# Kernel tuning notes

Hardware: AMD Instinct MI355X
Metric: run time of the kernel (lower is better)

The kernel has to match this reference:

```python
import jax, jax.numpy as jnp
import numpy as np

D_MODEL = 768
NHEAD = 12
HEAD_DIM = D_MODEL // NHEAD
B, L = 8, 1024


def setup_inputs() -> dict:
    key = jax.random.key(0)
    ks = jax.random.split(key, 10)
    s = 0.02  # init scale for weights
    return {
        "x": jax.random.normal(ks[0], (B, L, D_MODEL), dtype=jnp.float32),
        "pos": jax.random.normal(ks[1], (B, L, D_MODEL), dtype=jnp.float32),
        "qkv_w": jax.random.normal(ks[2], (3 * D_MODEL, D_MODEL), dtype=jnp.float32) * s,
        "qkv_b": jnp.zeros((3 * D_MODEL,), dtype=jnp.float32),
        "pq_w": jax.random.normal(ks[3], (D_MODEL, D_MODEL), dtype=jnp.float32) * s,
        "pq_b": jnp.zeros((D_MODEL,), dtype=jnp.float32),
        "pk_w": jax.random.normal(ks[4], (D_MODEL, D_MODEL), dtype=jnp.float32) * s,
        "pk_b": jnp.zeros((D_MODEL,), dtype=jnp.float32),
    }


def reference(x, pos, qkv_w, qkv_b, pq_w, pq_b, pk_w, pk_b):
    b, l, d = x.shape
    h, hd = NHEAD, HEAD_DIM

    qkv = x @ qkv_w.T + qkv_b  # (b, l, 3d)
    q, k, v = jnp.split(qkv, 3, axis=-1)
    # rearrange 'b l (h d) -> b l h d'
    q = q.reshape(b, l, h, hd)
    k = k.reshape(b, l, h, hd)
    v = v.reshape(b, l, h, hd)

    pq = (pos @ pq_w.T + pq_b).reshape(b, l, h, hd)
    pk = (pos @ pk_w.T + pk_b).reshape(b, l, h, hd)

    CC = jnp.einsum('bnhd,blhd->bhnl', q, k)
    CP = jnp.einsum('bnhd,blhd->bhnl', q, pq)
    PC = jnp.einsum('bnhd,blhd->bhnl', k, pk)

    # Faithful to source: only PC is scaled (operator precedence in original)
    scale = (3 * d) ** 0.5
    attn = jax.nn.softmax(CC + CP + PC / scale, axis=-1)

    out = jnp.einsum('bhnl,blhd->bnhd', attn, v)  # (b, n, h, hd)
    return out
```

## Files before the change

kernel.cpp:

```cpp
#include <hip/hip_runtime.h>
#include <hip/hip_bf16.h>

#define NHEAD 12
#define BATCH 8
#define SEQ 1024
#define LOG2E 1.4426950408889634f

typedef __bf16 bf16x8 __attribute__((ext_vector_type(8)));
typedef float  f32x4  __attribute__((ext_vector_type(4)));

#define WAITVM0 asm volatile("s_waitcnt vmcnt(0)" ::: "memory")

#define MFMA(A, B, C) __builtin_amdgcn_mfma_f32_16x16x32_bf16(A, B, C, 0, 0, 0)

__device__ __forceinline__ unsigned short f2bf(float f) {
    union { float f; unsigned u; } v; v.f = f;
    unsigned u = v.u;
    u += 0x7fff + ((u >> 16) & 1);
    return (unsigned short)(u >> 16);
}

__device__ __forceinline__ unsigned pkbf(float a, float b) {
    union { __hip_bfloat162 h; unsigned u; } cv;
    cv.h = __float22bfloat162_rn(make_float2(a, b));
    return cv.u;
}

__device__ __forceinline__ void gload_lds16(const void* g, void* l) {
    __builtin_amdgcn_global_load_lds(
        (const __attribute__((address_space(1))) unsigned*)g,
        (__attribute__((address_space(3))) unsigned*)l, 16, 0, 0);
}

#define SZ_X    6291456
#define SZ_QKVW 1769472
#define SZ_PW   589824
#define CONV_TOTAL 15532032

__global__ __launch_bounds__(256) void convert_kernel(
    const float* __restrict__ x, const float* __restrict__ pos,
    const float* __restrict__ qkv_w, const float* __restrict__ pq_w,
    const float* __restrict__ pk_w, unsigned short* __restrict__ dst)
{
    const size_t i4 = ((size_t)blockIdx.x * 256 + threadIdx.x) * 4;
    if (i4 >= CONV_TOTAL) return;
    const float* src; size_t off;
    if (i4 < SZ_X)                { src = x;     off = i4; }
    else if (i4 < 2 * SZ_X)       { src = pos;   off = i4 - SZ_X; }
    else if (i4 < 2 * SZ_X + SZ_QKVW) { src = qkv_w; off = i4 - 2 * SZ_X; }
    else if (i4 < 2 * SZ_X + SZ_QKVW + SZ_PW) { src = pq_w; off = i4 - 2 * SZ_X - SZ_QKVW; }
    else                          { src = pk_w;  off = i4 - 2 * SZ_X - SZ_QKVW - SZ_PW; }
    float4 v = *(const float4*)(src + off);
    ushort4 o;
    o.x = f2bf(v.x); o.y = f2bf(v.y); o.z = f2bf(v.z); o.w = f2bf(v.w);
    *(ushort4*)(dst + i4) = o;
}


#define PROJ_STAGE(K0, AS, BS) do {                                          \
    const int k0_ = (K0);                                                    \
    const unsigned short* asrc_; int acol_;                                  \
    if (g == 4)                    { asrc_ = posb; acol_ = k0_; }            \
    else if (g == 3 && k0_ >= 768) { asrc_ = posb; acol_ = k0_ - 768; }      \
    else                           { asrc_ = xb;   acol_ = k0_; }            \
    gload_lds16(asrc_ + (size_t)(m0 + r0) * 768 + acol_ + q0 * 8, &AS[base0]);\
    gload_lds16(asrc_ + (size_t)(m0 + r1) * 768 + acol_ + q1 * 8, &AS[base1]);\
    const unsigned short* wsrc_; int wro_, wco_;                             \
    if (g <= 2)       { wsrc_ = qkvw; wro_ = n0;        wco_ = k0_; }        \
    else if (g == 3) {                                                       \
        if (k0_ < 768) { wsrc_ = qkvw; wro_ = n0 - 1536; wco_ = k0_; }       \
        else           { wsrc_ = pqw;  wro_ = n0 - 2304; wco_ = k0_ - 768; } \
    } else            { wsrc_ = pkw;  wro_ = n0 - 3072; wco_ = k0_; }        \
    gload_lds16(wsrc_ + (size_t)(wro_ + r0) * 768 + wco_ + q0 * 8, &BS[base0]);\
    gload_lds16(wsrc_ + (size_t)(wro_ + r1) * 768 + wco_ + q1 * 8, &BS[base1]);\
} while (0)

#define PROJ_COMPUTE(AS, BS) do {                                            \
    bf16x8 af[4], bfr[4];                                                    \
    _Pragma("unroll")                                                        \
    for (int mt = 0; mt < 4; ++mt) {                                         \
        const int rr = wm + mt * 16 + col16;                                 \
        af[mt] = *(const bf16x8*)&AS[rr * 32 + ((quad ^ ((rr >> 1) & 3)) * 8)];\
    }                                                                        \
    _Pragma("unroll")                                                        \
    for (int nt = 0; nt < 4; ++nt) {                                         \
        const int rr = wn + nt * 16 + col16;                                 \
        bfr[nt] = *(const bf16x8*)&BS[rr * 32 + ((quad ^ ((rr >> 1) & 3)) * 8)];\
    }                                                                        \
    _Pragma("unroll")                                                        \
    for (int mt = 0; mt < 4; ++mt)                                           \
        _Pragma("unroll")                                                    \
        for (int nt = 0; nt < 4; ++nt)                                       \
            acc[mt][nt] = MFMA(af[mt], bfr[nt], acc[mt][nt]);                \
} while (0)

__global__ __launch_bounds__(256, 3) void proj_kernel(
    const unsigned short* __restrict__ xb, const unsigned short* __restrict__ posb,
    const unsigned short* __restrict__ qkvw, const unsigned short* __restrict__ pqw,
    const unsigned short* __restrict__ pkw,
    const float* __restrict__ qkv_b, const float* __restrict__ pq_b,
    const float* __restrict__ pk_b,
    unsigned short* __restrict__ Q2, unsigned short* __restrict__ K2,
    unsigned short* __restrict__ Vt, int band)
{
    __shared__ unsigned short As0[128 * 32];
    __shared__ unsigned short As1[128 * 32];
    __shared__ unsigned short Bs0[128 * 32];
    __shared__ unsigned short Bs1[128 * 32];

    const int id  = blockIdx.x;
    const int xcd = id & 7;
    const int idx = id >> 3;
    const int nt30 = (idx / band + 18) % 30;
    const int m0 = (xcd * band + idx % band) * 128;
    const int n0 = nt30 * 128;
    const int g  = n0 / 768;
    const int nk = (g == 3) ? 48 : 24;

    const int tid   = threadIdx.x;
    const int lane  = tid & 63;
    const int w     = tid >> 6;
    const int wm    = (w & 1) * 64;
    const int wn    = (w >> 1) * 64;
    const int quad  = lane >> 4;
    const int col16 = lane & 15;

    const int c0 = w * 64 + lane;
    const int c1 = c0 + 256;
    const int r0 = c0 >> 2, q0 = (c0 & 3) ^ ((c0 >> 3) & 3);
    const int r1 = c1 >> 2, q1 = (c1 & 3) ^ ((c1 >> 3) & 3);
    const int base0 = (w * 64) * 8;
    const int base1 = (w * 64 + 256) * 8;

    f32x4 acc[4][4];
    const f32x4 fzero = {0.f, 0.f, 0.f, 0.f};
#pragma unroll
    for (int mt = 0; mt < 4; ++mt)
#pragma unroll
        for (int nt = 0; nt < 4; ++nt) acc[mt][nt] = fzero;

    PROJ_STAGE(0, As0, Bs0);

    for (int kt = 0; kt < nk; kt += 2) {
        WAITVM0;
        __syncthreads();
        PROJ_STAGE((kt + 1) * 32, As1, Bs1);
        PROJ_COMPUTE(As0, Bs0);

        WAITVM0;
        __syncthreads();
        if (kt + 2 < nk) PROJ_STAGE((kt + 2) * 32, As0, Bs0);
        PROJ_COMPUTE(As1, Bs1);
    }

#pragma unroll
    for (int mt = 0; mt < 4; ++mt) {
        const int mbase = m0 + wm + mt * 16 + quad * 4;
#pragma unroll
        for (int nt = 0; nt < 4; ++nt) {
            const int n = n0 + wn + nt * 16 + col16;
            if (g == 2) {
                const int b = mbase >> 10, l0 = mbase & 1023;
                const int c = n - 1536, h = c >> 6, dd = c & 63;
                const float bias = qkv_b[n];
                uint2 pk;
                pk.x = pkbf(acc[mt][nt][0] + bias, acc[mt][nt][1] + bias);
                pk.y = pkbf(acc[mt][nt][2] + bias, acc[mt][nt][3] + bias);
                *(uint2*)&Vt[((size_t)(b * NHEAD + h) * 64 + dd) * 1024 + l0] = pk;
                continue;
            }
#pragma unroll
            for (int r = 0; r < 4; ++r) {
                const int m = mbase + r;
                const int b = m >> 10, l = m & 1023;
                float val = acc[mt][nt][r];
                if (g == 0) {
                    val = (val + qkv_b[n]) * LOG2E;
                    const int h = n >> 6, dd = n & 63;
                    Q2[((size_t)(b * NHEAD + h) * 1024 + l) * 128 + dd] = f2bf(val);
                } else if (g == 1) {
                    val = (val + qkv_b[n]) * (LOG2E / 48.0f);
                    const int c = n - 768, h = c >> 6, dd = c & 63;
                    Q2[((size_t)(b * NHEAD + h) * 1024 + l) * 128 + 64 + dd] = f2bf(val);
                } else if (g == 3) {
                    const int c = n - 2304;
                    val += qkv_b[n - 1536] + pq_b[c];
                    const int h = c >> 6, dd = c & 63;
                    K2[((size_t)(b * NHEAD + h) * 1024 + l) * 128 + dd] = f2bf(val);
                } else {
                    const int c = n - 3072;
                    val += pk_b[c];
                    const int h = c >> 6, dd = c & 63;
                    K2[((size_t)(b * NHEAD + h) * 1024 + l) * 128 + 64 + dd] = f2bf(val);
                }
            }
        }
    }
}


#define ATTN_STG(J0, KS, VS) do {                                            \
    const int j0_ = (J0);                                                    \
    gload_lds16(&K2[q2base + (size_t)(j0_ + kr0) * 128 + kc0 * 8], &KS[kbase0]);\
    gload_lds16(&K2[q2base + (size_t)(j0_ + kr1) * 128 + kc1 * 8], &KS[kbase1]);\
    gload_lds16(&Vt[vtbase + (size_t)vr * 1024 + j0_ + vc * 8],    &VS[vbase]);\
} while (0)

#define ATTN_PV(VS, PSR) do {                                                \
    bf16x8 bp0 = *(const bf16x8*)&PSR[w][col16][quad * 8];                   \
    bf16x8 bp1 = *(const bf16x8*)&PSR[w][16 + col16][quad * 8];              \
    _Pragma("unroll")                                                        \
    for (int c2 = 0; c2 < 4; ++c2) {                                         \
        const int rv = c2 * 16 + col16;                                      \
        bf16x8 av = *(const bf16x8*)&VS[rv * 32 + ((quad ^ ((rv >> 2) & 3)) * 8)];\
        o[0][c2] = MFMA(av, bp0, o[0][c2]);                                  \
        o[1][c2] = MFMA(av, bp1, o[1][c2]);                                  \
    }                                                                        \
} while (0)

#define ATTN_QK(KS, PSW) do {                                                \
    f32x4 st[2][2] = {{fzero, fzero}, {fzero, fzero}};                       \
    _Pragma("unroll")                                                        \
    for (int kk = 0; kk < 4; ++kk) {                                         \
        const int rrj0 = col16, rrj1 = 16 + col16;                           \
        bf16x8 kf0 = *(const bf16x8*)&KS[rrj0 * 128 + (((kk * 4 + quad) ^ (rrj0 & 15)) * 8)];\
        bf16x8 kf1 = *(const bf16x8*)&KS[rrj1 * 128 + (((kk * 4 + quad) ^ (rrj1 & 15)) * 8)];\
        _Pragma("unroll")                                                    \
        for (int qt = 0; qt < 2; ++qt) {                                     \
            st[0][qt] = MFMA(kf0, bq[qt][kk], st[0][qt]);                    \
            st[1][qt] = MFMA(kf1, bq[qt][kk], st[1][qt]);                    \
        }                                                                    \
    }                                                                        \
    _Pragma("unroll")                                                        \
    for (int qt = 0; qt < 2; ++qt) {                                         \
        float p0[4], p1[4], s = 0.f;                                         \
        _Pragma("unroll")                                                    \
        for (int r = 0; r < 4; ++r) {                                        \
            p0[r] = __builtin_amdgcn_exp2f(st[0][qt][r]);                    \
            p1[r] = __builtin_amdgcn_exp2f(st[1][qt][r]);                    \
            s += p0[r] + p1[r];                                              \
        }                                                                    \
        lsum[qt] += s;                                                       \
        uint2 w0, w1;                                                        \
        w0.x = pkbf(p0[0], p0[1]); w0.y = pkbf(p0[2], p0[3]);                \
        w1.x = pkbf(p1[0], p1[1]); w1.y = pkbf(p1[2], p1[3]);                \
        *(uint2*)&PSW[w][qt * 16 + col16][quad * 4]      = w0;               \
        *(uint2*)&PSW[w][qt * 16 + col16][16 + quad * 4] = w1;               \
    }                                                                        \
} while (0)

#define ATTN_PHASE(J, KQK, KST, VPV, VST, PSW, PSR, DOPV, DOST) do {         \
    WAITVM0;                                                                 \
    __syncthreads();                                                         \
    if (DOST) ATTN_STG(((J) + 1) * 32, KST, VST);                            \
    if (DOPV) ATTN_PV(VPV, PSR);                                             \
    ATTN_QK(KQK, PSW);                                                       \
} while (0)

__global__ __launch_bounds__(256, 3) void attn_kernel(
    const unsigned short* __restrict__ Q2, const unsigned short* __restrict__ K2,
    const unsigned short* __restrict__ Vt, float* __restrict__ out, int b0)
{
    __shared__ unsigned short K2sA[32 * 128];
    __shared__ unsigned short K2sB[32 * 128];
    __shared__ unsigned short VtX[64 * 32];
    __shared__ unsigned short VtY[64 * 32];
    __shared__ unsigned short VtZ[64 * 32];
    __shared__ unsigned short Ps0[4][32][40];
    __shared__ unsigned short Ps1[4][32][40];

    const int bh_l = blockIdx.x;
    const int b = b0 + bh_l / NHEAD, h = bh_l % NHEAD;
    const int tid   = threadIdx.x;
    const int lane  = tid & 63;
    const int w     = tid >> 6;
    const int quad  = lane >> 4;
    const int col16 = lane & 15;
    const int qbase = blockIdx.y * 128 + w * 32;

    const size_t q2base = (size_t)bh_l * 1024 * 128;
    const size_t vtbase = (size_t)bh_l * 64 * 1024;

    const int kL0 = w * 64 + lane, kL1 = kL0 + 256;
    const int kr0 = kL0 >> 4, kc0 = (kL0 & 15) ^ (kr0 & 15);
    const int kr1 = kL1 >> 4, kc1 = (kL1 & 15) ^ (kr1 & 15);
    const int vL  = w * 64 + lane;
    const int vr  = vL >> 2,  vc  = (vL & 3) ^ ((vL >> 4) & 3);
    const int kbase0 = (w * 64) * 8, kbase1 = (w * 64 + 256) * 8;
    const int vbase  = (w * 64) * 8;

    bf16x8 bq[2][4];
#pragma unroll
    for (int qt = 0; qt < 2; ++qt)
#pragma unroll
        for (int kk = 0; kk < 4; ++kk)
            bq[qt][kk] = *(const bf16x8*)&Q2[q2base +
                (size_t)(qbase + qt * 16 + col16) * 128 + kk * 32 + quad * 8];

    f32x4 o[2][4];
    const f32x4 fzero = {0.f, 0.f, 0.f, 0.f};
#pragma unroll
    for (int qt = 0; qt < 2; ++qt)
#pragma unroll
        for (int c2 = 0; c2 < 4; ++c2) o[qt][c2] = fzero;
    float lsum[2] = {0.f, 0.f};

    ATTN_STG(0, K2sA, VtX);

    ATTN_PHASE(0, K2sA, K2sB, VtZ, VtY, Ps0, Ps1, 0, 1);

    for (int j = 1; j < 31; j += 6) {
        ATTN_PHASE(j + 0, K2sB, K2sA, VtX, VtZ, Ps1, Ps0, 1, 1);
        ATTN_PHASE(j + 1, K2sA, K2sB, VtY, VtX, Ps0, Ps1, 1, 1);
        ATTN_PHASE(j + 2, K2sB, K2sA, VtZ, VtY, Ps1, Ps0, 1, 1);
        ATTN_PHASE(j + 3, K2sA, K2sB, VtX, VtZ, Ps0, Ps1, 1, 1);
        ATTN_PHASE(j + 4, K2sB, K2sA, VtY, VtX, Ps1, Ps0, 1, 1);
        ATTN_PHASE(j + 5, K2sA, K2sB, VtZ, VtY, Ps0, Ps1, 1, 1);
    }

    ATTN_PHASE(31, K2sB, K2sA, VtX, VtZ, Ps1, Ps0, 1, 0);

    ATTN_PV(VtY, Ps1);

#pragma unroll
    for (int qt = 0; qt < 2; ++qt) {
        lsum[qt] += __shfl_xor(lsum[qt], 16, 64);
        lsum[qt] += __shfl_xor(lsum[qt], 32, 64);
    }

#pragma unroll
    for (int qt = 0; qt < 2; ++qt) {
        const float inv = 1.0f / lsum[qt];
        const int q = qbase + qt * 16 + col16;
#pragma unroll
        for (int c2 = 0; c2 < 4; ++c2) {
#pragma unroll
            for (int r = 0; r < 4; ++r) {
                const int dd = c2 * 16 + quad * 4 + r;
                out[(((size_t)(b * 1024 + q)) * 12 + h) * 64 + dd] = o[qt][c2][r] * inv;
            }
        }
    }
}

extern "C" void kernel_launch(void* const* d_in, const int* in_sizes, int n_in,
                              void* d_out, int out_size, void* d_ws, size_t ws_size,
                              hipStream_t stream) {
    const float* x     = (const float*)d_in[0];
    const float* pos   = (const float*)d_in[1];
    const float* qkv_w = (const float*)d_in[2];
    const float* qkv_b = (const float*)d_in[3];
    const float* pq_w  = (const float*)d_in[4];
    const float* pq_b  = (const float*)d_in[5];
    const float* pk_w  = (const float*)d_in[6];
    const float* pk_b  = (const float*)d_in[7];
    float* out = (float*)d_out;

    unsigned short* ws   = (unsigned short*)d_ws;
    unsigned short* xb   = ws;
    unsigned short* posb = xb + SZ_X;
    unsigned short* qkvw = posb + SZ_X;
    unsigned short* pqw  = qkvw + SZ_QKVW;
    unsigned short* pkw  = pqw + SZ_PW;
    unsigned short* cbuf = pkw + SZ_PW;

    const size_t conv_bytes = (size_t)CONV_TOTAL * 2;
    const size_t per_batch  = (size_t)NHEAD * 1024 * 128 * 4
                            + (size_t)NHEAD * 64 * 1024 * 2;
    int cb = BATCH;
    while (cb > 1 && conv_bytes + (size_t)cb * per_batch > ws_size) cb >>= 1;

    unsigned short* Q2 = cbuf;
    unsigned short* K2 = Q2 + (size_t)cb * NHEAD * 1024 * 128;
    unsigned short* Vt = K2 + (size_t)cb * NHEAD * 1024 * 128;

    convert_kernel<<<(CONV_TOTAL / 4 + 255) / 256, 256, 0, stream>>>(
        x, pos, qkv_w, pq_w, pk_w, ws);

    for (int b0 = 0; b0 < BATCH; b0 += cb) {
        proj_kernel<<<dim3(cb * 240), 256, 0, stream>>>(
            xb + (size_t)b0 * 1024 * 768, posb + (size_t)b0 * 1024 * 768,
            qkvw, pqw, pkw, qkv_b, pq_b, pk_b, Q2, K2, Vt, cb);
        attn_kernel<<<dim3(cb * NHEAD, 8), 256, 0, stream>>>(Q2, K2, Vt, out, b0);
    }
}
```

Measured before the change: 243.6 us.

## Deepen prefetch pipelines to triple/quad buffering with partial vmcnt waits

The projection GEMM moves from double to triple buffering, keeping two tiles in flight and waiting with vmcnt(4) instead of draining all loads. The attention kernel prefetches two K/V tiles ahead, using three K buffers, four V buffers and a single P buffer, and waits with vmcnt(3). The goal is to hide global-to-LDS latency behind the MFMA work. In exchange the kernels use more LDS, which may lower occupancy, and the single P buffer depends on the per-phase barrier ordering to stay correct.

```diff
diff --git a/kernel.cpp b/kernel.cpp
--- a/kernel.cpp
+++ b/kernel.cpp
@@ -9,7 +9,7 @@
 typedef __bf16 bf16x8 __attribute__((ext_vector_type(8)));
 typedef float  f32x4  __attribute__((ext_vector_type(4)));
 
-#define WAITVM0 asm volatile("s_waitcnt vmcnt(0)" ::: "memory")
+#define VMWAIT(N) asm volatile("s_waitcnt vmcnt(" #N ")" ::: "memory")
 
 #define MFMA(A, B, C) __builtin_amdgcn_mfma_f32_16x16x32_bf16(A, B, C, 0, 0, 0)
 
@@ -105,8 +105,10 @@
 {
     __shared__ unsigned short As0[128 * 32];
     __shared__ unsigned short As1[128 * 32];
+    __shared__ unsigned short As2[128 * 32];
     __shared__ unsigned short Bs0[128 * 32];
     __shared__ unsigned short Bs1[128 * 32];
+    __shared__ unsigned short Bs2[128 * 32];
 
     const int id  = blockIdx.x;
     const int xcd = id & 7;
@@ -139,19 +141,23 @@
 #pragma unroll
         for (int nt = 0; nt < 4; ++nt) acc[mt][nt] = fzero;
 
-    PROJ_STAGE(0, As0, Bs0);
-
-    for (int kt = 0; kt < nk; kt += 2) {
-        WAITVM0;
-        __syncthreads();
-        PROJ_STAGE((kt + 1) * 32, As1, Bs1);
-        PROJ_COMPUTE(As0, Bs0);
-
-        WAITVM0;
-        __syncthreads();
-        if (kt + 2 < nk) PROJ_STAGE((kt + 2) * 32, As0, Bs0);
-        PROJ_COMPUTE(As1, Bs1);
-    }
+    PROJ_STAGE(0,  As0, Bs0);
+    PROJ_STAGE(32, As1, Bs1);
+
+    for (int s = 0; s + 5 < nk; s += 3) {
+        VMWAIT(4); __syncthreads();
+        PROJ_STAGE((s + 2) * 32, As2, Bs2); PROJ_COMPUTE(As0, Bs0);
+        VMWAIT(4); __syncthreads();
+        PROJ_STAGE((s + 3) * 32, As0, Bs0); PROJ_COMPUTE(As1, Bs1);
+        VMWAIT(4); __syncthreads();
+        PROJ_STAGE((s + 4) * 32, As1, Bs1); PROJ_COMPUTE(As2, Bs2);
+    }
+    VMWAIT(4); __syncthreads();
+    PROJ_STAGE((nk - 1) * 32, As2, Bs2); PROJ_COMPUTE(As0, Bs0);
+    VMWAIT(4); __syncthreads();
+    PROJ_COMPUTE(As1, Bs1);
+    VMWAIT(0); __syncthreads();
+    PROJ_COMPUTE(As2, Bs2);
 
 #pragma unroll
     for (int mt = 0; mt < 4; ++mt) {
@@ -206,9 +212,9 @@
     gload_lds16(&Vt[vtbase + (size_t)vr * 1024 + j0_ + vc * 8],    &VS[vbase]);\
 } while (0)
 
-#define ATTN_PV(VS, PSR) do {                                                \
-    bf16x8 bp0 = *(const bf16x8*)&PSR[w][col16][quad * 8];                   \
-    bf16x8 bp1 = *(const bf16x8*)&PSR[w][16 + col16][quad * 8];              \
+#define ATTN_PV(VS) do {                                                     \
+    bf16x8 bp0 = *(const bf16x8*)&Ps[w][col16][quad * 8];                    \
+    bf16x8 bp1 = *(const bf16x8*)&Ps[w][16 + col16][quad * 8];               \
     _Pragma("unroll")                                                        \
     for (int c2 = 0; c2 < 4; ++c2) {                                         \
         const int rv = c2 * 16 + col16;                                      \
@@ -218,7 +224,7 @@
     }                                                                        \
 } while (0)
 
-#define ATTN_QK(KS, PSW) do {                                                \
+#define ATTN_QK(KS) do {                                                     \
     f32x4 st[2][2] = {{fzero, fzero}, {fzero, fzero}};                       \
     _Pragma("unroll")                                                        \
     for (int kk = 0; kk < 4; ++kk) {                                         \
@@ -244,30 +250,31 @@
         uint2 w0, w1;                                                        \
         w0.x = pkbf(p0[0], p0[1]); w0.y = pkbf(p0[2], p0[3]);                \
         w1.x = pkbf(p1[0], p1[1]); w1.y = pkbf(p1[2], p1[3]);                \
-        *(uint2*)&PSW[w][qt * 16 + col16][quad * 4]      = w0;               \
-        *(uint2*)&PSW[w][qt * 16 + col16][16 + quad * 4] = w1;               \
+        *(uint2*)&Ps[w][qt * 16 + col16][quad * 4]      = w0;                \
+        *(uint2*)&Ps[w][qt * 16 + col16][16 + quad * 4] = w1;                \
     }                                                                        \
 } while (0)
 
-#define ATTN_PHASE(J, KQK, KST, VPV, VST, PSW, PSR, DOPV, DOST) do {         \
-    WAITVM0;                                                                 \
+#define ATTN_PH(J, KQ, KS, VP, VS, DOPV, DOST) do {                          \
+    VMWAIT(3);                                                               \
     __syncthreads();                                                         \
-    if (DOST) ATTN_STG(((J) + 1) * 32, KST, VST);                            \
-    if (DOPV) ATTN_PV(VPV, PSR);                                             \
-    ATTN_QK(KQK, PSW);                                                       \
+    if (DOST) ATTN_STG(((J) + 2) * 32, KS, VS);                              \
+    if (DOPV) ATTN_PV(VP);                                                   \
+    ATTN_QK(KQ);                                                             \
 } while (0)
 
 __global__ __launch_bounds__(256, 3) void attn_kernel(
     const unsigned short* __restrict__ Q2, const unsigned short* __restrict__ K2,
     const unsigned short* __restrict__ Vt, float* __restrict__ out, int b0)
 {
-    __shared__ unsigned short K2sA[32 * 128];
-    __shared__ unsigned short K2sB[32 * 128];
-    __shared__ unsigned short VtX[64 * 32];
-    __shared__ unsigned short VtY[64 * 32];
-    __shared__ unsigned short VtZ[64 * 32];
-    __shared__ unsigned short Ps0[4][32][40];
-    __shared__ unsigned short Ps1[4][32][40];
+    __shared__ unsigned short KA[32 * 128];
+    __shared__ unsigned short KB[32 * 128];
+    __shared__ unsigned short KC[32 * 128];
+    __shared__ unsigned short V0[64 * 32];
+    __shared__ unsigned short V1[64 * 32];
+    __shared__ unsigned short V2[64 * 32];
+    __shared__ unsigned short V3[64 * 32];
+    __shared__ unsigned short Ps[4][32][40];
 
     const int bh_l = blockIdx.x;
     const int b = b0 + bh_l / NHEAD, h = bh_l % NHEAD;
@@ -305,22 +312,35 @@
         for (int c2 = 0; c2 < 4; ++c2) o[qt][c2] = fzero;
     float lsum[2] = {0.f, 0.f};
 
-    ATTN_STG(0, K2sA, VtX);
-
-    ATTN_PHASE(0, K2sA, K2sB, VtZ, VtY, Ps0, Ps1, 0, 1);
-
-    for (int j = 1; j < 31; j += 6) {
-        ATTN_PHASE(j + 0, K2sB, K2sA, VtX, VtZ, Ps1, Ps0, 1, 1);
-        ATTN_PHASE(j + 1, K2sA, K2sB, VtY, VtX, Ps0, Ps1, 1, 1);
-        ATTN_PHASE(j + 2, K2sB, K2sA, VtZ, VtY, Ps1, Ps0, 1, 1);
-        ATTN_PHASE(j + 3, K2sA, K2sB, VtX, VtZ, Ps0, Ps1, 1, 1);
-        ATTN_PHASE(j + 4, K2sB, K2sA, VtY, VtX, Ps1, Ps0, 1, 1);
-        ATTN_PHASE(j + 5, K2sA, K2sB, VtZ, VtY, Ps0, Ps1, 1, 1);
-    }
-
-    ATTN_PHASE(31, K2sB, K2sA, VtX, VtZ, Ps1, Ps0, 1, 0);
-
-    ATTN_PV(VtY, Ps1);
+    ATTN_STG(0,  KA, V0);
+    ATTN_STG(32, KB, V1);
+
+    ATTN_PH(0,  KA, KC, V0, V2, 0, 1);
+    for (int j = 1; j <= 13; j += 12) {
+        ATTN_PH(j + 0,  KB, KA, V0, V3, 1, 1);
+        ATTN_PH(j + 1,  KC, KB, V1, V0, 1, 1);
+        ATTN_PH(j + 2,  KA, KC, V2, V1, 1, 1);
+        ATTN_PH(j + 3,  KB, KA, V3, V2, 1, 1);
+        ATTN_PH(j + 4,  KC, KB, V0, V3, 1, 1);
+        ATTN_PH(j + 5,  KA, KC, V1, V0, 1, 1);
+        ATTN_PH(j + 6,  KB, KA, V2, V1, 1, 1);
+        ATTN_PH(j + 7,  KC, KB, V3, V2, 1, 1);
+        ATTN_PH(j + 8,  KA, KC, V0, V3, 1, 1);
+        ATTN_PH(j + 9,  KB, KA, V1, V0, 1, 1);
+        ATTN_PH(j + 10, KC, KB, V2, V1, 1, 1);
+        ATTN_PH(j + 11, KA, KC, V3, V2, 1, 1);
+    }
+    ATTN_PH(25, KB, KA, V0, V3, 1, 1);
+    ATTN_PH(26, KC, KB, V1, V0, 1, 1);
+    ATTN_PH(27, KA, KC, V2, V1, 1, 1);
+    ATTN_PH(28, KB, KA, V3, V2, 1, 1);
+    ATTN_PH(29, KC, KB, V0, V3, 1, 1);
+    ATTN_PH(30, KA, KC, V1, V0, 1, 0);
+    VMWAIT(0);
+    __syncthreads();
+    ATTN_PV(V2);
+    ATTN_QK(KB);
+    ATTN_PV(V3);
 
 #pragma unroll
     for (int qt = 0; qt < 2; ++qt) {
```

Result: slower. 254.2 us (+4.4%).
